# Optimization experiments

Hardware: AMD Instinct MI355X
Metric: run time of the kernel (lower is better)

Reference implementation:

```python
import jax, jax.numpy as jnp
import numpy as np

D = 64        # GatedGraphConv out_channels
N_LAYERS = 5  # number of stacked convs


def setup_inputs() -> dict:
    key = jax.random.key(0)
    ks = jax.random.split(key, 16)
    N, E, G = 100000, 1600000, 64
    s = 0.1
    inp = {
        'conv_weight': jax.random.normal(ks[0], (N_LAYERS, D, D), jnp.float32) * s,
        'gru_w_ih':    jax.random.normal(ks[1], (N_LAYERS, 3 * D, D), jnp.float32) * s,
        'gru_w_hh':    jax.random.normal(ks[2], (N_LAYERS, 3 * D, D), jnp.float32) * s,
        'gru_b_ih':    jax.random.normal(ks[3], (N_LAYERS, 3 * D), jnp.float32) * s,
        'gru_b_hh':    jax.random.normal(ks[4], (N_LAYERS, 3 * D), jnp.float32) * s,
        'fc1_w': jax.random.normal(ks[5], (32, D), jnp.float32) * s,
        'fc1_b': jax.random.normal(ks[6], (32,), jnp.float32) * s,
        'fc2_w': jax.random.normal(ks[7], (16, 32), jnp.float32) * s,
        'fc2_b': jax.random.normal(ks[8], (16,), jnp.float32) * s,
        'fc3_w': jax.random.normal(ks[9], (1, 16), jnp.float32) * s,
        'fc3_b': jax.random.normal(ks[10], (1,), jnp.float32) * s,
        'edge_index': jax.random.randint(ks[11], (2, E), 0, N, jnp.int64 if jax.config.jax_enable_x64 else jnp.int32),
        'batch': jnp.sort(jax.random.randint(ks[12], (N,), 0, G, jnp.int32)),
        'num_nodes': N,
        'num_graphs': G,
    }
    return inp


def _gru_cell(m, h, w_ih, w_hh, b_ih, b_hh):
    # torch.nn.GRUCell math; m: [N,D] input, h: [N,D] hidden
    gi = m @ w_ih.T + b_ih   # [N, 3D]
    gh = h @ w_hh.T + b_hh   # [N, 3D]
    i_r, i_z, i_n = jnp.split(gi, 3, axis=1)
    h_r, h_z, h_n = jnp.split(gh, 3, axis=1)
    r = jax.nn.sigmoid(i_r + h_r)
    z = jax.nn.sigmoid(i_z + h_z)
    n = jnp.tanh(i_n + r * h_n)
    return (1.0 - z) * n + z * h


def reference(conv_weight, gru_w_ih, gru_w_hh, gru_b_ih, gru_b_hh,
              fc1_w, fc1_b, fc2_w, fc2_b, fc3_w, fc3_b,
              edge_index, batch, num_nodes, num_graphs):
    src, dst = edge_index[0], edge_index[1]  # source_to_target flow
    # initial node features: zeros [N,8] zero-padded to D by GatedGraphConv
    x0 = jnp.zeros((num_nodes, D), jnp.float32)

    def step(x, params):
        w, wih, whh, bih, bhh = params
        m = x @ w                                        # [N, D]
        agg = jax.ops.segment_sum(m[src], dst, num_segments=num_nodes)  # scatter-add
        return _gru_cell(agg, x, wih, whh, bih, bhh), None

    x, _ = jax.lax.scan(step, x0,
                        (conv_weight, gru_w_ih, gru_w_hh, gru_b_ih, gru_b_hh))

    # scatter_add pooling over batch -> [num_graphs, D]
    g = jax.ops.segment_sum(x, batch, num_segments=num_graphs)
    h = jax.nn.elu(g @ fc1_w.T + fc1_b)
    h = jax.nn.elu(h @ fc2_w.T + fc2_b)
    return h @ fc3_w.T + fc3_b  # [num_graphs, 1]
```

## Files before the change

kernel.cpp:

```cpp
#include <hip/hip_runtime.h>
#include <math.h>

typedef _Float16 f16x2 __attribute__((ext_vector_type(2)));
typedef _Float16 f16x4 __attribute__((ext_vector_type(4)));
typedef _Float16 f16x8 __attribute__((ext_vector_type(8)));
typedef float f32x4 __attribute__((ext_vector_type(4)));

#define CBITS 10
#define FCHUNK 4096
#define MATSZ 13056
#define SEGSZ 2176
#define TABN 512
__device__ __forceinline__ int woff(int row) { return 64 * row + 8 * (row >> 1); }

__device__ __forceinline__ float sigmoidf_(float v) {
  return 1.0f / (1.0f + __expf(-v));
}
__device__ __forceinline__ float tanhf_(float v) {
  v = fminf(fmaxf(v, -15.f), 15.f);
  float e = __expf(2.f * v);
  return (e - 1.f) / (e + 1.f);
}
__device__ __forceinline__ float eluf_(float v) { return v > 0.f ? v : (__expf(v) - 1.f); }

__global__ __launch_bounds__(256) void wprep_kernel(const float* __restrict__ conv_w,
                                                    const float* __restrict__ w_ih,
                                                    const float* __restrict__ whh,
                                                    _Float16* __restrict__ wcS,
                                                    _Float16* __restrict__ whhS) {
  __shared__ float sWt[64 * 68];
  __shared__ float sI[48 * 64];
  const int t = threadIdx.x;
  if (blockIdx.x < 12) {
    const int l = 2 + (blockIdx.x >> 2);
    const int j0 = (blockIdx.x & 3) * 48;
    const float* W = conv_w + (size_t)l * 4096;
    const float* wi = w_ih + (size_t)l * 12288;
    _Float16* out = wcS + (size_t)l * MATSZ;
    for (int i = t; i < 4096; i += 256) sWt[(i & 63) * 68 + (i >> 6)] = W[i];
    for (int i = t; i < 3072; i += 256) sI[i] = wi[j0 * 64 + i];
    __syncthreads();
#pragma unroll
    for (int r = 0; r < 3; ++r) {
      int u = t + 256 * r;
      int j = u >> 4, cg = (u & 15) * 4;
      float4 a = {0.f, 0.f, 0.f, 0.f};
      for (int k = 0; k < 64; ++k) {
        float4 w = *(const float4*)(sWt + k * 68 + cg);
        float s = sI[j * 64 + k];
        a.x += w.x * s; a.y += w.y * s; a.z += w.z * s; a.w += w.w * s;
      }
      int row = j0 + j;
      f16x4 hv;
      hv[0] = (_Float16)a.x; hv[1] = (_Float16)a.y;
      hv[2] = (_Float16)a.z; hv[3] = (_Float16)a.w;
      *(f16x4*)(out + woff(row) + cg) = hv;
    }
  } else {
    int idx = (blockIdx.x - 12) * 256 + t;
    if (idx >= 9216) return;
    int l = 2 + idx / 3072, rem = idx % 3072;
    int r = rem >> 4, c4 = (rem & 15) * 4;
    float4 v = *(const float4*)(whh + (size_t)l * 12288 + r * 64 + c4);
    f16x4 hv;
    hv[0] = (_Float16)v.x; hv[1] = (_Float16)v.y;
    hv[2] = (_Float16)v.z; hv[3] = (_Float16)v.w;
    *(f16x4*)(whhS + (size_t)l * MATSZ + woff(r) + c4) = hv;
  }
}

__global__ __launch_bounds__(256) void bucket_hist_kernel(const int* __restrict__ dst,
                                                          int* __restrict__ bh, int E) {
  __shared__ int h[128];
  const int t = threadIdx.x;
  if (t < 128) h[t] = 0;
  __syncthreads();
  for (int e = blockIdx.x * 256 + t; e < E; e += gridDim.x * 256)
    atomicAdd(&h[dst[e] >> CBITS], 1);
  __syncthreads();
  if (t < 128 && h[t]) atomicAdd(&bh[t * 16], h[t]);
}

__global__ __launch_bounds__(128) void bucket_scan_kernel(int* __restrict__ bh, int nbk,
                                                          int* __restrict__ boffs, int E,
                                                          float* __restrict__ gbuf, int gn) {
  __shared__ int s[128];
  const int t = threadIdx.x;
  for (int i = t; i < gn; i += 128) gbuf[i] = 0.f;
  int v = (t < nbk) ? bh[t * 16] : 0;
  s[t] = v;
  __syncthreads();
  for (int o = 1; o < 128; o <<= 1) {
    int a = (t >= o) ? s[t - o] : 0;
    __syncthreads();
    s[t] += a;
    __syncthreads();
  }
  if (t < nbk) {
    int ex = s[t] - v;
    boffs[t] = ex;
    bh[t * 16] = ex;
  }
  if (t == 0) boffs[nbk] = E;
}

__global__ __launch_bounds__(256) void bucket_fill_kernel(const int* __restrict__ src,
                                                          const int* __restrict__ dst,
                                                          int* __restrict__ bcur,
                                                          unsigned* __restrict__ pairs, int E) {
  __shared__ uint2 staged[FCHUNK];
  __shared__ int h[128], lbase[128], gbase[128], lcur[128];
  const int t = threadIdx.x;
  const int e0 = blockIdx.x * FCHUNK;
  int cnt = E - e0;
  if (cnt > FCHUNK) cnt = FCHUNK;
  if (t < 128) h[t] = 0;
  __syncthreads();
  for (int i = t; i < cnt; i += 256) atomicAdd(&h[dst[e0 + i] >> CBITS], 1);
  __syncthreads();
  if (t < 128) lcur[t] = h[t];
  __syncthreads();
  for (int o = 1; o < 128; o <<= 1) {
    int a = 0;
    if (t < 128 && t >= o) a = lcur[t - o];
    __syncthreads();
    if (t < 128) lcur[t] += a;
    __syncthreads();
  }
  if (t < 128) {
    int ex = lcur[t] - h[t];
    lbase[t] = ex;
    if (h[t]) gbase[t] = atomicAdd(&bcur[t * 16], h[t]);
    lcur[t] = ex;
  }
  __syncthreads();
  for (int i = t; i < cnt; i += 256) {
    int d = dst[e0 + i];
    int b = d >> CBITS;
    int p = atomicAdd(&lcur[b], 1);
    staged[p] = make_uint2((unsigned)src[e0 + i], (unsigned)d);
  }
  __syncthreads();
  for (int i = t; i < cnt; i += 256) {
    uint2 pr = staged[i];
    int b = (int)(pr.y >> CBITS);
    pairs[gbase[b] + (i - lbase[b])] = (pr.x << CBITS) | (pr.y & ((1u << CBITS) - 1));
  }
}

__global__ __launch_bounds__(256) void csr_build_kernel(const unsigned* __restrict__ pairs,
                                                        const int* __restrict__ boffs,
                                                        int* __restrict__ offs,
                                                        int* __restrict__ srcs,
                                                        unsigned short* __restrict__ deg16,
                                                        int N, int E) {
  const int b = blockIdx.x, t = threadIdx.x;
  const int nbase = b << CBITS;
  __shared__ int deg[1024];
  __shared__ int ssc[256];
  for (int i = t; i < 1024; i += 256) deg[i] = 0;
  __syncthreads();
  const int beg = boffs[b], end = boffs[b + 1];
  for (int e = beg + t; e < end; e += 256) atomicAdd(&deg[pairs[e] & 1023], 1);
  __syncthreads();
  int d0 = deg[4 * t], d1 = deg[4 * t + 1], d2 = deg[4 * t + 2], d3 = deg[4 * t + 3];
  int s = d0 + d1 + d2 + d3;
  ssc[t] = s;
  __syncthreads();
  for (int o = 1; o < 256; o <<= 1) {
    int a = (t >= o) ? ssc[t - o] : 0;
    __syncthreads();
    ssc[t] += a;
    __syncthreads();
  }
  int base = beg + ssc[t] - s;
  int c0 = base, c1 = c0 + d0, c2 = c1 + d1, c3 = c2 + d2;
  if (nbase + 4 * t + 0 < N) { offs[nbase + 4 * t + 0] = c0; deg16[nbase + 4 * t + 0] = (unsigned short)d0; }
  if (nbase + 4 * t + 1 < N) { offs[nbase + 4 * t + 1] = c1; deg16[nbase + 4 * t + 1] = (unsigned short)d1; }
  if (nbase + 4 * t + 2 < N) { offs[nbase + 4 * t + 2] = c2; deg16[nbase + 4 * t + 2] = (unsigned short)d2; }
  if (nbase + 4 * t + 3 < N) { offs[nbase + 4 * t + 3] = c3; deg16[nbase + 4 * t + 3] = (unsigned short)d3; }
  deg[4 * t] = c0; deg[4 * t + 1] = c1; deg[4 * t + 2] = c2; deg[4 * t + 3] = c3;
  if (b == 0 && t == 0) offs[N] = E;
  if (b == 0 && t < 64) srcs[E + t] = 0;
  __syncthreads();
  for (int e = beg + t; e < end; e += 256) {
    unsigned p = pairs[e];
    int pos = atomicAdd(&deg[p & 1023], 1);
    srcs[pos] = (int)(p >> CBITS);
  }
}

__global__ __launch_bounds__(256) void l01tab_kernel(const float* __restrict__ conv_w,
                                                     const float* __restrict__ w_ih,
                                                     const float* __restrict__ w_hh,
                                                     const float* __restrict__ b_ih,
                                                     const float* __restrict__ b_hh,
                                                     _Float16* __restrict__ tab) {
  __shared__ float sh1[64], st[64], su[192], scons[256];
  const int t = threadIdx.x;
  if (t < 64) {
    float r = sigmoidf_(b_ih[t] + b_hh[t]);
    float z = sigmoidf_(b_ih[64 + t] + b_hh[64 + t]);
    float n = tanhf_(b_ih[128 + t] + r * b_hh[128 + t]);
    sh1[t] = (1.f - z) * n;
  }
  __syncthreads();
  if (t < 64) {
    const float* W1 = conv_w + 4096;
    float a = 0.f;
    for (int c = 0; c < 64; ++c) a += sh1[c] * W1[c * 64 + t];
    st[t] = a;
  }
  __syncthreads();
  if (t < 192) {
    const float* wih1 = w_ih + 12288;
    const float* whh1 = w_hh + 12288;
    float uacc = 0.f, sg = 0.f;
    for (int k = 0; k < 64; ++k) {
      uacc += wih1[t * 64 + k] * st[k];
      sg += whh1[t * 64 + k] * sh1[k];
    }
    su[t] = uacc;
    const float* bi1 = b_ih + 192;
    const float* bh1 = b_hh + 192;
    if (t < 128) {
      scons[t] = sg + bi1[t] + bh1[t];
    } else {
      scons[t] = bi1[t];
      scons[t + 64] = sg + bh1[t];
    }
  }
  __syncthreads();
  for (int idx = t; idx < TABN * 64; idx += 256) {
    int dgi = idx >> 6, j = idx & 63;
    float dg = (float)dgi;
    float r = sigmoidf_(dg * su[j] + scons[j]);
    float z = sigmoidf_(dg * su[64 + j] + scons[64 + j]);
    float n = tanhf_(dg * su[128 + j] + scons[128 + j] + r * scons[192 + j]);
    tab[idx] = (_Float16)(n + z * (sh1[j] - n));
  }
}

__global__ __launch_bounds__(256) void agg2_kernel(const _Float16* __restrict__ tab,
                                                   const unsigned short* __restrict__ deg16,
                                                   const int* __restrict__ offs,
                                                   const int* __restrict__ srcs,
                                                   _Float16* __restrict__ aggh, int N) {
  int wave = threadIdx.x >> 6, lane = threadIdx.x & 63;
  int v = blockIdx.x * 4 + wave;
  if (v >= N) return;
  const int beg = offs[v], end = offs[v + 1];
  const int deg = end - beg;
  const int og = lane >> 3;
  const int lp = lane & 7;
  f16x8 acc = {};
  for (int base = 0; base < deg; base += 64) {
    const int cnt = min(64, deg - base);
    const int cnt8 = (cnt + 7) & ~7;
    int sidx = 0;
    if (lane < cnt8) sidx = srcs[beg + base + lane];
    int s0 = __shfl(sidx, og);
    int d0 = min((int)deg16[s0], TABN - 1);
    f16x8 cur = *(const f16x8*)(tab + d0 * 64 + lp * 8);
    int e = 0;
    for (; e + 8 < cnt; e += 8) {
      int sn = __shfl(sidx, e + 8 + og);
      int dn = min((int)deg16[sn], TABN - 1);
      f16x8 nxt = *(const f16x8*)(tab + dn * 64 + lp * 8);
      acc += cur;
      cur = nxt;
    }
    if (e + og < cnt) acc += cur;
  }
#pragma unroll
  for (int off = 8; off < 64; off <<= 1) {
    union { f16x8 h; int i[4]; } a, b;
    a.h = acc;
#pragma unroll
    for (int w = 0; w < 4; ++w) b.i[w] = __shfl_xor(a.i[w], off);
    acc += b.h;
  }
  if (og == 0) *(f16x8*)(aggh + (size_t)v * 64 + lp * 8) = acc;
}

__global__ __launch_bounds__(256) void agg_kernel(const _Float16* __restrict__ xh,
                                                  const int* __restrict__ offs,
                                                  const int* __restrict__ srcs,
                                                  _Float16* __restrict__ aggh, int N) {
  int wave = threadIdx.x >> 6, lane = threadIdx.x & 63;
  int v = blockIdx.x * 4 + wave;
  if (v >= N) return;
  const int beg = offs[v], end = offs[v + 1];
  const int deg = end - beg;
  const int og = lane >> 3;
  const int lp = lane & 7;
  f16x8 acc = {};
  for (int base = 0; base < deg; base += 64) {
    const int cnt = min(64, deg - base);
    const int cnt8 = (cnt + 7) & ~7;
    int sidx = 0;
    if (lane < cnt8) sidx = srcs[beg + base + lane];
    int s0 = __shfl(sidx, og);
    f16x8 cur = *(const f16x8*)(xh + (size_t)s0 * 64 + lp * 8);
    int e = 0;
    for (; e + 8 < cnt; e += 8) {
      int sn = __shfl(sidx, e + 8 + og);
      f16x8 nxt = *(const f16x8*)(xh + (size_t)sn * 64 + lp * 8);
      acc += cur;
      cur = nxt;
    }
    if (e + og < cnt) acc += cur;
  }
#pragma unroll
  for (int off = 8; off < 64; off <<= 1) {
    union { f16x8 h; int i[4]; } a, b;
    a.h = acc;
#pragma unroll
    for (int w = 0; w < 4; ++w) b.i[w] = __shfl_xor(a.i[w], off);
    acc += b.h;
  }
  if (og == 0) *(f16x8*)(aggh + (size_t)v * 64 + lp * 8) = acc;
}

template <bool TABH>
__device__ __forceinline__ void gru_body(const _Float16* __restrict__ aggh,
                                         const _Float16* __restrict__ xh_in,
                                         const unsigned short* __restrict__ deg16,
                                         const _Float16* __restrict__ tab,
                                         _Float16* __restrict__ xh_out,
                                         const _Float16* __restrict__ wcS,
                                         const _Float16* __restrict__ whhS,
                                         const float* __restrict__ b_ih,
                                         const float* __restrict__ b_hh,
                                         int N, int tiles) {
  __shared__ _Float16 sW[2 * 3 * SEGSZ];
  const int t = threadIdx.x;
  const int half = blockIdx.x & 1;
  for (int i = t; i < 1632; i += 256) {
    int mat = (i >= 816) ? 1 : 0;
    int rem = i - mat * 816;
    int seg = rem / 272;
    int u = rem % 272;
    const _Float16* srcp = (mat ? whhS : wcS) + woff(half * 32 + seg * 64) + u * 8;
    *(f16x8*)(sW + (mat * 3 + seg) * SEGSZ + u * 8) = *(const f16x8*)srcp;
  }
  __syncthreads();
  const int wave = t >> 6, lane = t & 63;
  const int q = lane >> 4, c = lane & 15;
  float bRZ[2], bZZ[2], bIN[2], bHN[2];
#pragma unroll
  for (int p = 0; p < 2; ++p) {
    int d = (half * 2 + p) * 16 + c;
    bRZ[p] = b_ih[d] + b_hh[d];
    bZZ[p] = b_ih[64 + d] + b_hh[64 + d];
    bIN[p] = b_ih[128 + d];
    bHN[p] = b_hh[128 + d];
  }
  f16x8 idf[2];
#pragma unroll
  for (int p = 0; p < 2; ++p) {
    int tgt = p * 16 + c - q * 8;
#pragma unroll
    for (int j = 0; j < 8; ++j) idf[p][j] = (j == tgt) ? (_Float16)1.0f : (_Float16)0.0f;
  }
#pragma unroll 1
  for (int tile = blockIdx.x >> 1; tile < tiles; tile += gridDim.x >> 1) {
    const int nb0 = tile * 64 + wave * 16;
    const size_t rowbase = (size_t)(nb0 + c) * 64;
    f16x8 aA[2], aH[2];
    if (TABH) {
      int dg = min((int)deg16[nb0 + c], TABN - 1);
#pragma unroll
      for (int ks = 0; ks < 2; ++ks) {
        aA[ks] = *(const f16x8*)(aggh + rowbase + ks * 32 + q * 8);
        aH[ks] = *(const f16x8*)(tab + dg * 64 + ks * 32 + q * 8);
      }
    } else {
#pragma unroll
      for (int ks = 0; ks < 2; ++ks) {
        aA[ks] = *(const f16x8*)(aggh + rowbase + ks * 32 + q * 8);
        aH[ks] = *(const f16x8*)(xh_in + rowbase + ks * 32 + q * 8);
      }
    }
    f32x4 aR[2], aZ[2], aN[2], aHNa[2], aHO[2];
#pragma unroll
    for (int p = 0; p < 2; ++p) {
      aR[p] = (f32x4){bRZ[p], bRZ[p], bRZ[p], bRZ[p]};
      aZ[p] = (f32x4){bZZ[p], bZZ[p], bZZ[p], bZZ[p]};
      aN[p] = (f32x4){bIN[p], bIN[p], bIN[p], bIN[p]};
      aHNa[p] = (f32x4){bHN[p], bHN[p], bHN[p], bHN[p]};
      aHO[p] = (f32x4){0.f, 0.f, 0.f, 0.f};
    }
#pragma unroll
    for (int ks = 0; ks < 2; ++ks) {
      const int colo = ks * 32 + q * 8;
#pragma unroll
      for (int p = 0; p < 2; ++p) {
        const int lr = p * 16 + c;
        const int ro = 64 * lr + 8 * (lr >> 1);
        f16x8 bWr = *(const f16x8*)(sW + 0 * SEGSZ + ro + colo);
        f16x8 bWz = *(const f16x8*)(sW + 1 * SEGSZ + ro + colo);
        f16x8 bWn = *(const f16x8*)(sW + 2 * SEGSZ + ro + colo);
        f16x8 bHr = *(const f16x8*)(sW + 3 * SEGSZ + ro + colo);
        f16x8 bHz = *(const f16x8*)(sW + 4 * SEGSZ + ro + colo);
        f16x8 bHn = *(const f16x8*)(sW + 5 * SEGSZ + ro + colo);
        aR[p] = __builtin_amdgcn_mfma_f32_16x16x32_f16(aA[ks], bWr, aR[p], 0, 0, 0);
        aR[p] = __builtin_amdgcn_mfma_f32_16x16x32_f16(aH[ks], bHr, aR[p], 0, 0, 0);
        aZ[p] = __builtin_amdgcn_mfma_f32_16x16x32_f16(aA[ks], bWz, aZ[p], 0, 0, 0);
        aZ[p] = __builtin_amdgcn_mfma_f32_16x16x32_f16(aH[ks], bHz, aZ[p], 0, 0, 0);
        aN[p] = __builtin_amdgcn_mfma_f32_16x16x32_f16(aA[ks], bWn, aN[p], 0, 0, 0);
        aHNa[p] = __builtin_amdgcn_mfma_f32_16x16x32_f16(aH[ks], bHn, aHNa[p], 0, 0, 0);
      }
    }
#pragma unroll
    for (int p = 0; p < 2; ++p)
      aHO[p] = __builtin_amdgcn_mfma_f32_16x16x32_f16(aH[half], idf[p], aHO[p], 0, 0, 0);
#pragma unroll
    for (int p = 0; p < 2; ++p) {
      int d = (half * 2 + p) * 16 + c;
#pragma unroll
      for (int r = 0; r < 4; ++r) {
        int node = nb0 + q * 4 + r;
        if (node < N) {
          float rr = sigmoidf_(aR[p][r]);
          float zz = sigmoidf_(aZ[p][r]);
          float nn = tanhf_(aN[p][r] + rr * aHNa[p][r]);
          float out = nn + zz * (aHO[p][r] - nn);
          xh_out[(size_t)node * 64 + d] = (_Float16)out;
        }
      }
    }
  }
}

__global__ __launch_bounds__(256) void gru_kernel(const _Float16* __restrict__ aggh,
                                                  const _Float16* __restrict__ xh_in,
                                                  _Float16* __restrict__ xh_out,
                                                  const _Float16* __restrict__ wcS,
                                                  const _Float16* __restrict__ whhS,
                                                  const float* __restrict__ b_ih,
                                                  const float* __restrict__ b_hh,
                                                  int N, int tiles) {
  gru_body<false>(aggh, xh_in, nullptr, nullptr, xh_out, wcS, whhS, b_ih, b_hh, N, tiles);
}

__global__ __launch_bounds__(256) void gru2_kernel(const _Float16* __restrict__ aggh,
                                                   const unsigned short* __restrict__ deg16,
                                                   const _Float16* __restrict__ tab,
                                                   _Float16* __restrict__ xh_out,
                                                   const _Float16* __restrict__ wcS,
                                                   const _Float16* __restrict__ whhS,
                                                   const float* __restrict__ b_ih,
                                                   const float* __restrict__ b_hh,
                                                   int N, int tiles) {
  gru_body<true>(aggh, nullptr, deg16, tab, xh_out, wcS, whhS, b_ih, b_hh, N, tiles);
}

__global__ __launch_bounds__(256) void pool_kernel(const _Float16* __restrict__ xh,
                                                   const int* __restrict__ batch,
                                                   float* __restrict__ g, int N) {
  int wave = threadIdx.x >> 6, lane = threadIdx.x & 63;
  int n0 = blockIdx.x * 64 + wave * 16;
  if (n0 >= N) return;
  int end = n0 + 16;
  if (end > N) end = N;
  int cur = batch[n0];
  float acc = 0.f;
  for (int n = n0; n < end; ++n) {
    int b = batch[n];
    if (b != cur) {
      atomicAdd(&g[(size_t)cur * 64 + lane], acc);
      acc = 0.f;
      cur = b;
    }
    acc += (float)xh[(size_t)n * 64 + lane];
  }
  atomicAdd(&g[(size_t)cur * 64 + lane], acc);
}

__global__ __launch_bounds__(256) void mlp_kernel(const float* __restrict__ g,
                                                  const float* __restrict__ w1,
                                                  const float* __restrict__ b1,
                                                  const float* __restrict__ w2,
                                                  const float* __restrict__ b2,
                                                  const float* __restrict__ w3,
                                                  const float* __restrict__ b3,
                                                  float* __restrict__ out, int G) {
  __shared__ float sG[64 * 64];
  __shared__ float sH1[64 * 32];
  __shared__ float sH2[64 * 16];
  int t = threadIdx.x;
  for (int i = t; i < G * 64; i += 256) sG[i] = g[i];
  __syncthreads();
  for (int o = t; o < G * 32; o += 256) {
    int gi = o >> 5, i = o & 31;
    float a = b1[i];
    for (int k = 0; k < 64; ++k) a += sG[gi * 64 + k] * w1[i * 64 + k];
    sH1[gi * 32 + i] = eluf_(a);
  }
  __syncthreads();
  for (int o = t; o < G * 16; o += 256) {
    int gi = o >> 4, i = o & 15;
    float a = b2[i];
    for (int k = 0; k < 32; ++k) a += sH1[gi * 32 + k] * w2[i * 32 + k];
    sH2[gi * 16 + i] = eluf_(a);
  }
  __syncthreads();
  for (int o = t; o < G; o += 256) {
    float a = b3[0];
    for (int k = 0; k < 16; ++k) a += sH2[o * 16 + k] * w3[k];
    out[o] = a;
  }
}

extern "C" void kernel_launch(void* const* d_in, const int* in_sizes, int n_in,
                              void* d_out, int out_size, void* d_ws, size_t ws_size,
                              hipStream_t stream) {
  const float* conv_w = (const float*)d_in[0];
  const float* w_ih = (const float*)d_in[1];
  const float* w_hh = (const float*)d_in[2];
  const float* b_ih = (const float*)d_in[3];
  const float* b_hh = (const float*)d_in[4];
  const float* fc1_w = (const float*)d_in[5];
  const float* fc1_b = (const float*)d_in[6];
  const float* fc2_w = (const float*)d_in[7];
  const float* fc2_b = (const float*)d_in[8];
  const float* fc3_w = (const float*)d_in[9];
  const float* fc3_b = (const float*)d_in[10];
  const int* ei = (const int*)d_in[11];
  const int* batch = (const int*)d_in[12];
  const int N = in_sizes[12];
  const int E = in_sizes[11] / 2;
  const int G = out_size;
  const int* src = ei;
  const int* dst = ei + E;
  const int nbk = (N + 1023) >> CBITS;
  const int tiles = (N + 63) / 64;
  const int Npad = tiles * 64;

  char* ws = (char*)d_ws;
  size_t off = 0;
  auto alloc = [&](size_t bytes) -> void* {
    void* p = ws + off;
    off += (bytes + 255) & ~(size_t)255;
    return p;
  };
  _Float16* xhA = (_Float16*)alloc((size_t)Npad * 64 * 2);
  _Float16* xhB = (_Float16*)alloc((size_t)Npad * 64 * 2);
  _Float16* aggh = (_Float16*)alloc((size_t)Npad * 64 * 2);
  _Float16* wcS = (_Float16*)alloc((size_t)5 * MATSZ * 2);
  _Float16* whhS = (_Float16*)alloc((size_t)5 * MATSZ * 2);
  _Float16* h2tab = (_Float16*)alloc((size_t)TABN * 64 * 2);
  float* gbuf = (float*)alloc((size_t)G * 64 * 4);
  int* offs = (int*)alloc((size_t)(N + 1) * 4);
  int* srcs = (int*)alloc((size_t)(E + 64) * 4);
  unsigned short* deg16 = (unsigned short*)alloc((size_t)Npad * 2);
  unsigned* pairs = (unsigned*)alloc((size_t)E * 4);
  int* bh = (int*)alloc(128 * 16 * 4);
  int* boffs = (int*)alloc(129 * 4);

  hipMemsetAsync(bh, 0, 128 * 16 * 4, stream);
  bucket_hist_kernel<<<256, 256, 0, stream>>>(dst, bh, E);
  bucket_scan_kernel<<<1, 128, 0, stream>>>(bh, nbk, boffs, E, gbuf, G * 64);
  bucket_fill_kernel<<<(E + FCHUNK - 1) / FCHUNK, 256, 0, stream>>>(src, dst, bh, pairs, E);
  csr_build_kernel<<<nbk, 256, 0, stream>>>(pairs, boffs, offs, srcs, deg16, N, E);

  wprep_kernel<<<48, 256, 0, stream>>>(conv_w, w_ih, w_hh, wcS, whhS);
  l01tab_kernel<<<1, 256, 0, stream>>>(conv_w, w_ih, w_hh, b_ih, b_hh, h2tab);

  agg2_kernel<<<(N + 3) / 4, 256, 0, stream>>>(h2tab, deg16, offs, srcs, aggh, N);
  gru2_kernel<<<768, 256, 0, stream>>>(aggh, deg16, h2tab, xhA, wcS + 2 * MATSZ,
                                       whhS + 2 * MATSZ, b_ih + 2 * 192, b_hh + 2 * 192,
                                       N, tiles);
  _Float16* cur = xhA;
  _Float16* nxt = xhB;
  for (int l = 3; l < 5; ++l) {
    agg_kernel<<<(N + 3) / 4, 256, 0, stream>>>(cur, offs, srcs, aggh, N);
    gru_kernel<<<768, 256, 0, stream>>>(aggh, cur, nxt, wcS + (size_t)l * MATSZ,
                                        whhS + (size_t)l * MATSZ, b_ih + (size_t)l * 192,
                                        b_hh + (size_t)l * 192, N, tiles);
    _Float16* tmp = cur; cur = nxt; nxt = tmp;
  }

  pool_kernel<<<(N + 63) / 64, 256, 0, stream>>>(cur, batch, gbuf, N);
  mlp_kernel<<<1, 256, 0, stream>>>(gbuf, fc1_w, fc1_b, fc2_w, fc2_b, fc3_w, fc3_b,
                                    (float*)d_out, G);
}
```

Before: 411.6 us.

## Cut kernel launches by merging CSR build, weight prep, and pool+MLP stages

Replaces the memset, global-atomic histogram and single-block scan with a per-chunk histogram written to a matrix. Each fill and CSR block now recomputes its prefix sums from that matrix, so the later kernels read the offsets directly. The layer-0/1 table build and gbuf zeroing move into an extra wprep block, and pooling plus the MLP head become one kernel where the last-finishing block runs the MLP. This removes several launches and serial tiny kernels, but every fill block must redundantly read the full nfb×128 histogram.

```diff
diff --git a/kernel.cpp b/kernel.cpp
--- a/kernel.cpp
+++ b/kernel.cpp
@@ -23,13 +23,151 @@
 }
 __device__ __forceinline__ float eluf_(float v) { return v > 0.f ? v : (__expf(v) - 1.f); }
 
+__global__ __launch_bounds__(256) void hist_kernel(const int* __restrict__ dst,
+                                                   int* __restrict__ bh, int E) {
+  __shared__ int h[128];
+  const int t = threadIdx.x;
+  if (t < 128) h[t] = 0;
+  __syncthreads();
+  const int e0 = blockIdx.x * FCHUNK;
+  int cnt = E - e0;
+  if (cnt > FCHUNK) cnt = FCHUNK;
+  for (int i = t; i < cnt; i += 256) atomicAdd(&h[dst[e0 + i] >> CBITS], 1);
+  __syncthreads();
+  if (t < 128) bh[blockIdx.x * 128 + t] = h[t];
+}
+
+__global__ __launch_bounds__(256) void bucket_fill_kernel(const int* __restrict__ src,
+                                                          const int* __restrict__ dst,
+                                                          const int* __restrict__ bh,
+                                                          unsigned* __restrict__ pairs,
+                                                          int E, int nfb) {
+  __shared__ uint2 staged[FCHUNK];
+  __shared__ int h[128], lbase[128], gbase[128], lcur[128], cs[128];
+  const int t = threadIdx.x;
+  const int k = blockIdx.x;
+  int tot = 0, own = 0, myh = 0;
+  if (t < 128) {
+    for (int kk = 0; kk < nfb; ++kk) {
+      int v = bh[kk * 128 + t];
+      if (kk < k) own += v;
+      if (kk == k) myh = v;
+      tot += v;
+    }
+    cs[t] = tot;
+    h[t] = myh;
+  }
+  __syncthreads();
+  for (int o = 1; o < 128; o <<= 1) {
+    int a = (t < 128 && t >= o) ? cs[t - o] : 0;
+    __syncthreads();
+    if (t < 128) cs[t] += a;
+    __syncthreads();
+  }
+  if (t < 128) {
+    gbase[t] = (cs[t] - tot) + own;
+    lcur[t] = h[t];
+  }
+  __syncthreads();
+  for (int o = 1; o < 128; o <<= 1) {
+    int a = (t < 128 && t >= o) ? lcur[t - o] : 0;
+    __syncthreads();
+    if (t < 128) lcur[t] += a;
+    __syncthreads();
+  }
+  if (t < 128) {
+    int ex = lcur[t] - h[t];
+    lbase[t] = ex;
+    lcur[t] = ex;
+  }
+  __syncthreads();
+  const int e0 = k * FCHUNK;
+  int cnt = E - e0;
+  if (cnt > FCHUNK) cnt = FCHUNK;
+  for (int i = t; i < cnt; i += 256) {
+    int d = dst[e0 + i];
+    int b = d >> CBITS;
+    int p = atomicAdd(&lcur[b], 1);
+    staged[p] = make_uint2((unsigned)src[e0 + i], (unsigned)d);
+  }
+  __syncthreads();
+  for (int i = t; i < cnt; i += 256) {
+    uint2 pr = staged[i];
+    int b = (int)(pr.y >> CBITS);
+    pairs[gbase[b] + (i - lbase[b])] = (pr.x << CBITS) | (pr.y & ((1u << CBITS) - 1));
+  }
+}
+
+__global__ __launch_bounds__(256) void csr_build_kernel(const unsigned* __restrict__ pairs,
+                                                        const int* __restrict__ bh,
+                                                        int* __restrict__ offs,
+                                                        int* __restrict__ srcs,
+                                                        unsigned short* __restrict__ deg16,
+                                                        int N, int E, int nfb) {
+  const int b = blockIdx.x, t = threadIdx.x;
+  const int nbase = b << CBITS;
+  __shared__ int deg[1024];
+  __shared__ int ssc[256];
+  __shared__ int cs[128];
+  if (t < 128) {
+    int a = 0;
+    for (int kk = 0; kk < nfb; ++kk) a += bh[kk * 128 + t];
+    cs[t] = a;
+  }
+  __syncthreads();
+  for (int o = 1; o < 128; o <<= 1) {
+    int a = (t < 128 && t >= o) ? cs[t - o] : 0;
+    __syncthreads();
+    if (t < 128) cs[t] += a;
+    __syncthreads();
+  }
+  const int beg = (b > 0) ? cs[b - 1] : 0;
+  const int end = cs[b];
+  __syncthreads();
+  for (int i = t; i < 1024; i += 256) deg[i] = 0;
+  __syncthreads();
+  for (int e = beg + t; e < end; e += 256) atomicAdd(&deg[pairs[e] & 1023], 1);
+  __syncthreads();
+  int d0 = deg[4 * t], d1 = deg[4 * t + 1], d2 = deg[4 * t + 2], d3 = deg[4 * t + 3];
+  int s = d0 + d1 + d2 + d3;
+  ssc[t] = s;
+  __syncthreads();
+  for (int o = 1; o < 256; o <<= 1) {
+    int a = (t >= o) ? ssc[t - o] : 0;
+    __syncthreads();
+    ssc[t] += a;
+    __syncthreads();
+  }
+  int base = beg + ssc[t] - s;
+  int c0 = base, c1 = c0 + d0, c2 = c1 + d1, c3 = c2 + d2;
+  if (nbase + 4 * t + 0 < N) { offs[nbase + 4 * t + 0] = c0; deg16[nbase + 4 * t + 0] = (unsigned short)d0; }
+  if (nbase + 4 * t + 1 < N) { offs[nbase + 4 * t + 1] = c1; deg16[nbase + 4 * t + 1] = (unsigned short)d1; }
+  if (nbase + 4 * t + 2 < N) { offs[nbase + 4 * t + 2] = c2; deg16[nbase + 4 * t + 2] = (unsigned short)d2; }
+  if (nbase + 4 * t + 3 < N) { offs[nbase + 4 * t + 3] = c3; deg16[nbase + 4 * t + 3] = (unsigned short)d3; }
+  deg[4 * t] = c0; deg[4 * t + 1] = c1; deg[4 * t + 2] = c2; deg[4 * t + 3] = c3;
+  if (b == 0 && t == 0) offs[N] = E;
+  if (b == 0 && t < 64) srcs[E + t] = 0;
+  __syncthreads();
+  for (int e = beg + t; e < end; e += 256) {
+    unsigned p = pairs[e];
+    int pos = atomicAdd(&deg[p & 1023], 1);
+    srcs[pos] = (int)(p >> CBITS);
+  }
+}
+
 __global__ __launch_bounds__(256) void wprep_kernel(const float* __restrict__ conv_w,
                                                     const float* __restrict__ w_ih,
                                                     const float* __restrict__ whh,
+                                                    const float* __restrict__ b_ih,
+                                                    const float* __restrict__ b_hh,
                                                     _Float16* __restrict__ wcS,
-                                                    _Float16* __restrict__ whhS) {
+                                                    _Float16* __restrict__ whhS,
+                                                    _Float16* __restrict__ tab,
+                                                    float* __restrict__ gbuf, int gn,
+                                                    int* __restrict__ done) {
   __shared__ float sWt[64 * 68];
   __shared__ float sI[48 * 64];
+  __shared__ float sh1[64], st[64], su[192], scons[256];
   const int t = threadIdx.x;
   if (blockIdx.x < 12) {
     const int l = 2 + (blockIdx.x >> 2);
@@ -56,7 +194,7 @@
       hv[2] = (_Float16)a.z; hv[3] = (_Float16)a.w;
       *(f16x4*)(out + woff(row) + cg) = hv;
     }
-  } else {
+  } else if (blockIdx.x < 48) {
     int idx = (blockIdx.x - 12) * 256 + t;
     if (idx >= 9216) return;
     int l = 2 + idx / 3072, rem = idx % 3072;
@@ -66,178 +204,50 @@
     hv[0] = (_Float16)v.x; hv[1] = (_Float16)v.y;
     hv[2] = (_Float16)v.z; hv[3] = (_Float16)v.w;
     *(f16x4*)(whhS + (size_t)l * MATSZ + woff(r) + c4) = hv;
-  }
-}
-
-__global__ __launch_bounds__(256) void bucket_hist_kernel(const int* __restrict__ dst,
-                                                          int* __restrict__ bh, int E) {
-  __shared__ int h[128];
-  const int t = threadIdx.x;
-  if (t < 128) h[t] = 0;
-  __syncthreads();
-  for (int e = blockIdx.x * 256 + t; e < E; e += gridDim.x * 256)
-    atomicAdd(&h[dst[e] >> CBITS], 1);
-  __syncthreads();
-  if (t < 128 && h[t]) atomicAdd(&bh[t * 16], h[t]);
-}
-
-__global__ __launch_bounds__(128) void bucket_scan_kernel(int* __restrict__ bh, int nbk,
-                                                          int* __restrict__ boffs, int E,
-                                                          float* __restrict__ gbuf, int gn) {
-  __shared__ int s[128];
-  const int t = threadIdx.x;
-  for (int i = t; i < gn; i += 128) gbuf[i] = 0.f;
-  int v = (t < nbk) ? bh[t * 16] : 0;
-  s[t] = v;
-  __syncthreads();
-  for (int o = 1; o < 128; o <<= 1) {
-    int a = (t >= o) ? s[t - o] : 0;
-    __syncthreads();
-    s[t] += a;
-    __syncthreads();
-  }
-  if (t < nbk) {
-    int ex = s[t] - v;
-    boffs[t] = ex;
-    bh[t * 16] = ex;
-  }
-  if (t == 0) boffs[nbk] = E;
-}
-
-__global__ __launch_bounds__(256) void bucket_fill_kernel(const int* __restrict__ src,
-                                                          const int* __restrict__ dst,
-                                                          int* __restrict__ bcur,
-                                                          unsigned* __restrict__ pairs, int E) {
-  __shared__ uint2 staged[FCHUNK];
-  __shared__ int h[128], lbase[128], gbase[128], lcur[128];
-  const int t = threadIdx.x;
-  const int e0 = blockIdx.x * FCHUNK;
-  int cnt = E - e0;
-  if (cnt > FCHUNK) cnt = FCHUNK;
-  if (t < 128) h[t] = 0;
-  __syncthreads();
-  for (int i = t; i < cnt; i += 256) atomicAdd(&h[dst[e0 + i] >> CBITS], 1);
-  __syncthreads();
-  if (t < 128) lcur[t] = h[t];
-  __syncthreads();
-  for (int o = 1; o < 128; o <<= 1) {
-    int a = 0;
-    if (t < 128 && t >= o) a = lcur[t - o];
-    __syncthreads();
-    if (t < 128) lcur[t] += a;
-    __syncthreads();
-  }
-  if (t < 128) {
-    int ex = lcur[t] - h[t];
-    lbase[t] = ex;
-    if (h[t]) gbase[t] = atomicAdd(&bcur[t * 16], h[t]);
-    lcur[t] = ex;
-  }
-  __syncthreads();
-  for (int i = t; i < cnt; i += 256) {
-    int d = dst[e0 + i];
-    int b = d >> CBITS;
-    int p = atomicAdd(&lcur[b], 1);
-    staged[p] = make_uint2((unsigned)src[e0 + i], (unsigned)d);
-  }
-  __syncthreads();
-  for (int i = t; i < cnt; i += 256) {
-    uint2 pr = staged[i];
-    int b = (int)(pr.y >> CBITS);
-    pairs[gbase[b] + (i - lbase[b])] = (pr.x << CBITS) | (pr.y & ((1u << CBITS) - 1));
-  }
-}
-
-__global__ __launch_bounds__(256) void csr_build_kernel(const unsigned* __restrict__ pairs,
-                                                        const int* __restrict__ boffs,
-                                                        int* __restrict__ offs,
-                                                        int* __restrict__ srcs,
-                                                        unsigned short* __restrict__ deg16,
-                                                        int N, int E) {
-  const int b = blockIdx.x, t = threadIdx.x;
-  const int nbase = b << CBITS;
-  __shared__ int deg[1024];
-  __shared__ int ssc[256];
-  for (int i = t; i < 1024; i += 256) deg[i] = 0;
-  __syncthreads();
-  const int beg = boffs[b], end = boffs[b + 1];
-  for (int e = beg + t; e < end; e += 256) atomicAdd(&deg[pairs[e] & 1023], 1);
-  __syncthreads();
-  int d0 = deg[4 * t], d1 = deg[4 * t + 1], d2 = deg[4 * t + 2], d3 = deg[4 * t + 3];
-  int s = d0 + d1 + d2 + d3;
-  ssc[t] = s;
-  __syncthreads();
-  for (int o = 1; o < 256; o <<= 1) {
-    int a = (t >= o) ? ssc[t - o] : 0;
-    __syncthreads();
-    ssc[t] += a;
-    __syncthreads();
-  }
-  int base = beg + ssc[t] - s;
-  int c0 = base, c1 = c0 + d0, c2 = c1 + d1, c3 = c2 + d2;
-  if (nbase + 4 * t + 0 < N) { offs[nbase + 4 * t + 0] = c0; deg16[nbase + 4 * t + 0] = (unsigned short)d0; }
-  if (nbase + 4 * t + 1 < N) { offs[nbase + 4 * t + 1] = c1; deg16[nbase + 4 * t + 1] = (unsigned short)d1; }
-  if (nbase + 4 * t + 2 < N) { offs[nbase + 4 * t + 2] = c2; deg16[nbase + 4 * t + 2] = (unsigned short)d2; }
-  if (nbase + 4 * t + 3 < N) { offs[nbase + 4 * t + 3] = c3; deg16[nbase + 4 * t + 3] = (unsigned short)d3; }
-  deg[4 * t] = c0; deg[4 * t + 1] = c1; deg[4 * t + 2] = c2; deg[4 * t + 3] = c3;
-  if (b == 0 && t == 0) offs[N] = E;
-  if (b == 0 && t < 64) srcs[E + t] = 0;
-  __syncthreads();
-  for (int e = beg + t; e < end; e += 256) {
-    unsigned p = pairs[e];
-    int pos = atomicAdd(&deg[p & 1023], 1);
-    srcs[pos] = (int)(p >> CBITS);
-  }
-}
-
-__global__ __launch_bounds__(256) void l01tab_kernel(const float* __restrict__ conv_w,
-                                                     const float* __restrict__ w_ih,
-                                                     const float* __restrict__ w_hh,
-                                                     const float* __restrict__ b_ih,
-                                                     const float* __restrict__ b_hh,
-                                                     _Float16* __restrict__ tab) {
-  __shared__ float sh1[64], st[64], su[192], scons[256];
-  const int t = threadIdx.x;
-  if (t < 64) {
-    float r = sigmoidf_(b_ih[t] + b_hh[t]);
-    float z = sigmoidf_(b_ih[64 + t] + b_hh[64 + t]);
-    float n = tanhf_(b_ih[128 + t] + r * b_hh[128 + t]);
-    sh1[t] = (1.f - z) * n;
-  }
-  __syncthreads();
-  if (t < 64) {
-    const float* W1 = conv_w + 4096;
-    float a = 0.f;
-    for (int c = 0; c < 64; ++c) a += sh1[c] * W1[c * 64 + t];
-    st[t] = a;
-  }
-  __syncthreads();
-  if (t < 192) {
-    const float* wih1 = w_ih + 12288;
-    const float* whh1 = w_hh + 12288;
-    float uacc = 0.f, sg = 0.f;
-    for (int k = 0; k < 64; ++k) {
-      uacc += wih1[t * 64 + k] * st[k];
-      sg += whh1[t * 64 + k] * sh1[k];
-    }
-    su[t] = uacc;
-    const float* bi1 = b_ih + 192;
-    const float* bh1 = b_hh + 192;
-    if (t < 128) {
-      scons[t] = sg + bi1[t] + bh1[t];
-    } else {
-      scons[t] = bi1[t];
-      scons[t + 64] = sg + bh1[t];
-    }
-  }
-  __syncthreads();
-  for (int idx = t; idx < TABN * 64; idx += 256) {
-    int dgi = idx >> 6, j = idx & 63;
-    float dg = (float)dgi;
-    float r = sigmoidf_(dg * su[j] + scons[j]);
-    float z = sigmoidf_(dg * su[64 + j] + scons[64 + j]);
-    float n = tanhf_(dg * su[128 + j] + scons[128 + j] + r * scons[192 + j]);
-    tab[idx] = (_Float16)(n + z * (sh1[j] - n));
+  } else {
+    for (int i = t; i < gn; i += 256) gbuf[i] = 0.f;
+    if (t == 0) *done = 0;
+    if (t < 64) {
+      float r = sigmoidf_(b_ih[t] + b_hh[t]);
+      float z = sigmoidf_(b_ih[64 + t] + b_hh[64 + t]);
+      float n = tanhf_(b_ih[128 + t] + r * b_hh[128 + t]);
+      sh1[t] = (1.f - z) * n;
+    }
+    __syncthreads();
+    if (t < 64) {
+      const float* W1 = conv_w + 4096;
+      float a = 0.f;
+      for (int c = 0; c < 64; ++c) a += sh1[c] * W1[c * 64 + t];
+      st[t] = a;
+    }
+    __syncthreads();
+    if (t < 192) {
+      const float* wih1 = w_ih + 12288;
+      const float* whh1 = whh + 12288;
+      float uacc = 0.f, sg = 0.f;
+      for (int k = 0; k < 64; ++k) {
+        uacc += wih1[t * 64 + k] * st[k];
+        sg += whh1[t * 64 + k] * sh1[k];
+      }
+      su[t] = uacc;
+      const float* bi1 = b_ih + 192;
+      const float* bh1 = b_hh + 192;
+      if (t < 128) {
+        scons[t] = sg + bi1[t] + bh1[t];
+      } else {
+        scons[t] = bi1[t];
+        scons[t + 64] = sg + bh1[t];
+      }
+    }
+    __syncthreads();
+    for (int idx = t; idx < TABN * 64; idx += 256) {
+      int dgi = idx >> 6, j = idx & 63;
+      float dg = (float)dgi;
+      float r = sigmoidf_(dg * su[j] + scons[j]);
+      float z = sigmoidf_(dg * su[64 + j] + scons[64 + j]);
+      float n = tanhf_(dg * su[128 + j] + scons[128 + j] + r * scons[192 + j]);
+      tab[idx] = (_Float16)(n + z * (sh1[j] - n));
+    }
   }
 }
 
@@ -456,41 +466,49 @@
   gru_body<true>(aggh, nullptr, deg16, tab, xh_out, wcS, whhS, b_ih, b_hh, N, tiles);
 }
 
-__global__ __launch_bounds__(256) void pool_kernel(const _Float16* __restrict__ xh,
-                                                   const int* __restrict__ batch,
-                                                   float* __restrict__ g, int N) {
+__global__ __launch_bounds__(256) void poolmlp_kernel(const _Float16* __restrict__ xh,
+                                                      const int* __restrict__ batch,
+                                                      float* __restrict__ g,
+                                                      int* __restrict__ done,
+                                                      const float* __restrict__ w1,
+                                                      const float* __restrict__ b1,
+                                                      const float* __restrict__ w2,
+                                                      const float* __restrict__ b2,
+                                                      const float* __restrict__ w3,
+                                                      const float* __restrict__ b3,
+                                                      float* __restrict__ out, int N, int G) {
   int wave = threadIdx.x >> 6, lane = threadIdx.x & 63;
   int n0 = blockIdx.x * 64 + wave * 16;
-  if (n0 >= N) return;
-  int end = n0 + 16;
-  if (end > N) end = N;
-  int cur = batch[n0];
-  float acc = 0.f;
-  for (int n = n0; n < end; ++n) {
-    int b = batch[n];
-    if (b != cur) {
-      atomicAdd(&g[(size_t)cur * 64 + lane], acc);
-      acc = 0.f;
-      cur = b;
-    }
-    acc += (float)xh[(size_t)n * 64 + lane];
-  }
-  atomicAdd(&g[(size_t)cur * 64 + lane], acc);
-}
-
-__global__ __launch_bounds__(256) void mlp_kernel(const float* __restrict__ g,
-                                                  const float* __restrict__ w1,
-                                                  const float* __restrict__ b1,
-                                                  const float* __restrict__ w2,
-                                                  const float* __restrict__ b2,
-                                                  const float* __restrict__ w3,
-                                                  const float* __restrict__ b3,
-                                                  float* __restrict__ out, int G) {
+  if (n0 < N) {
+    int end = n0 + 16;
+    if (end > N) end = N;
+    int cur = batch[n0];
+    float acc = 0.f;
+    for (int n = n0; n < end; ++n) {
+      int b = batch[n];
+      if (b != cur) {
+        atomicAdd(&g[(size_t)cur * 64 + lane], acc);
+        acc = 0.f;
+        cur = b;
+      }
+      acc += (float)xh[(size_t)n * 64 + lane];
+    }
+    atomicAdd(&g[(size_t)cur * 64 + lane], acc);
+  }
+  __threadfence();
+  __syncthreads();
+  __shared__ int lastFlag;
+  if (threadIdx.x == 0)
+    lastFlag = (__hip_atomic_fetch_add(done, 1, __ATOMIC_ACQ_REL, __HIP_MEMORY_SCOPE_AGENT)
+                == (int)gridDim.x - 1);
+  __syncthreads();
+  if (!lastFlag) return;
   __shared__ float sG[64 * 64];
   __shared__ float sH1[64 * 32];
   __shared__ float sH2[64 * 16];
   int t = threadIdx.x;
-  for (int i = t; i < G * 64; i += 256) sG[i] = g[i];
+  for (int i = t; i < G * 64; i += 256)
+    sG[i] = __hip_atomic_load(&g[i], __ATOMIC_RELAXED, __HIP_MEMORY_SCOPE_AGENT);
   __syncthreads();
   for (int o = t; o < G * 32; o += 256) {
     int gi = o >> 5, i = o & 31;
@@ -534,6 +552,7 @@
   const int G = out_size;
   const int* src = ei;
   const int* dst = ei + E;
+  const int nfb = (E + FCHUNK - 1) / FCHUNK;
   const int nbk = (N + 1023) >> CBITS;
   const int tiles = (N + 63) / 64;
   const int Npad = tiles * 64;
@@ -556,17 +575,15 @@
   int* srcs = (int*)alloc((size_t)(E + 64) * 4);
   unsigned short* deg16 = (unsigned short*)alloc((size_t)Npad * 2);
   unsigned* pairs = (unsigned*)alloc((size_t)E * 4);
-  int* bh = (int*)alloc(128 * 16 * 4);
-  int* boffs = (int*)alloc(129 * 4);
-
-  hipMemsetAsync(bh, 0, 128 * 16 * 4, stream);
-  bucket_hist_kernel<<<256, 256, 0, stream>>>(dst, bh, E);
-  bucket_scan_kernel<<<1, 128, 0, stream>>>(bh, nbk, boffs, E, gbuf, G * 64);
-  bucket_fill_kernel<<<(E + FCHUNK - 1) / FCHUNK, 256, 0, stream>>>(src, dst, bh, pairs, E);
-  csr_build_kernel<<<nbk, 256, 0, stream>>>(pairs, boffs, offs, srcs, deg16, N, E);
-
-  wprep_kernel<<<48, 256, 0, stream>>>(conv_w, w_ih, w_hh, wcS, whhS);
-  l01tab_kernel<<<1, 256, 0, stream>>>(conv_w, w_ih, w_hh, b_ih, b_hh, h2tab);
+  int* bh = (int*)alloc((size_t)nfb * 128 * 4);
+  int* done = (int*)alloc(256);
+
+  hist_kernel<<<nfb, 256, 0, stream>>>(dst, bh, E);
+  bucket_fill_kernel<<<nfb, 256, 0, stream>>>(src, dst, bh, pairs, E, nfb);
+  csr_build_kernel<<<nbk, 256, 0, stream>>>(pairs, bh, offs, srcs, deg16, N, E, nfb);
+
+  wprep_kernel<<<49, 256, 0, stream>>>(conv_w, w_ih, w_hh, b_ih, b_hh, wcS, whhS,
+                                       h2tab, gbuf, G * 64, done);
 
   agg2_kernel<<<(N + 3) / 4, 256, 0, stream>>>(h2tab, deg16, offs, srcs, aggh, N);
   gru2_kernel<<<768, 256, 0, stream>>>(aggh, deg16, h2tab, xhA, wcS + 2 * MATSZ,
@@ -582,7 +599,7 @@
     _Float16* tmp = cur; cur = nxt; nxt = tmp;
   }
 
-  pool_kernel<<<(N + 63) / 64, 256, 0, stream>>>(cur, batch, gbuf, N);
-  mlp_kernel<<<1, 256, 0, stream>>>(gbuf, fc1_w, fc1_b, fc2_w, fc2_b, fc3_w, fc3_b,
-                                    (float*)d_out, G);
-}
+  poolmlp_kernel<<<(N + 63) / 64, 256, 0, stream>>>(cur, batch, gbuf, done,
+                                                    fc1_w, fc1_b, fc2_w, fc2_b, fc3_w, fc3_b,
+                                                    (float*)d_out, N, G);
+}
```

Measured after the change: 629.3 us. 52.9% more time.
